# Optimization experiments

Measured on AMD Instinct MI355X. Metric: run time of the kernel, lower is better.

## Reference

```python
import jax, jax.numpy as jnp
import numpy as np

EPS = 1e-5

def layer_norm(x, g, b):
    m = jnp.mean(x, axis=-1, keepdims=True)
    v = jnp.mean((x - m) ** 2, axis=-1, keepdims=True)
    return (x - m) / jnp.sqrt(v + EPS) * g + b

def setup_inputs() -> dict:
    key = jax.random.key(0)
    ks = jax.random.split(key, 12)
    B, S, D, H = 8, 2048, 1024, 2048
    std = 0.02
    inp = {
        "x_embeddings": jax.random.normal(ks[0], (B, S, D), jnp.float32),
        # weights stored [in, out]; torch Linear computes x @ W.T + b
        "wq": jax.random.normal(ks[1], (D, D), jnp.float32) * std,
        "bq": jnp.zeros((D,), jnp.float32),
        "wk": jax.random.normal(ks[2], (D, D), jnp.float32) * std,
        "bk": jnp.zeros((D,), jnp.float32),
        "wv": jax.random.normal(ks[3], (D, D), jnp.float32) * std,
        "bv": jnp.zeros((D,), jnp.float32),
        "w0": jax.random.normal(ks[4], (D, D), jnp.float32) * std,
        "b0": jnp.zeros((D,), jnp.float32),
        "w1": jax.random.normal(ks[5], (D, H), jnp.float32) * std,
        "b1": jnp.zeros((H,), jnp.float32),
        "ln_g": jnp.ones((H,), jnp.float32),
        "ln_b": jnp.zeros((H,), jnp.float32),
        "w2": jax.random.normal(ks[6], (H, D), jnp.float32) * std,
        "b2": jnp.zeros((D,), jnp.float32),
        "n1_g": jnp.ones((D,), jnp.float32),
        "n1_b": jnp.zeros((D,), jnp.float32),
        "n2_g": jnp.ones((D,), jnp.float32),
        "n2_b": jnp.zeros((D,), jnp.float32),
    }
    return inp

def reference(x_embeddings, wq, bq, wk, bk, wv, bv, w0, b0, w1, b1, ln_g, ln_b, w2, b2, n1_g, n1_b, n2_g, n2_b):
    x = x_embeddings
    q = x @ wq + bq  # [B,S,D]
    k = x @ wk + bk
    v = x @ wv + bv
    # NOTE: original has NO 1/sqrt(d) scaling and NO causal mask in forward
    scores = jnp.einsum("bsd,btd->bst", q, k)
    probs = jax.nn.softmax(scores, axis=-1)
    attn = jnp.einsum("bst,btd->bsd", probs, v)
    e = layer_norm(x + attn, n1_g, n1_b) @ w0 + b0
    # MLP: Linear -> LeakyReLU -> LayerNorm(2048) -> Dropout(eval: identity) -> Linear
    h = jax.nn.leaky_relu(e @ w1 + b1, negative_slope=0.01)
    h = layer_norm(h, ln_g, ln_b)
    logits = h @ w2 + b2
    return layer_norm(jax.nn.leaky_relu(logits + e, negative_slope=0.01), n2_g, n2_b)
```

## Files before the change

kernel.cpp:

```cpp
#include <hip/hip_runtime.h>
#include <cstdint>
#include <cmath>

typedef unsigned short u16;
typedef __attribute__((ext_vector_type(4))) float f32x4;
typedef __attribute__((ext_vector_type(8))) _Float16 f16x8;

#define GPTR(p) ((__attribute__((address_space(1))) void*)(uintptr_t)(p))
#define LPTR(p) ((__attribute__((address_space(3))) void*)(uint32_t)(uintptr_t)(p))

__device__ __forceinline__ u16 f2h(float f) {
  const _Float16 h = (_Float16)f;
  return __builtin_bit_cast(u16, h);
}
__device__ __forceinline__ float h2f(u16 v) {
  return (float)__builtin_bit_cast(_Float16, v);
}

__global__ __launch_bounds__(256) void fill_kernel(float* __restrict__ p, float v, long n) {
  const long i = (long)blockIdx.x * 256 + threadIdx.x;
  if (i < n) p[i] = v;
}

__global__ __launch_bounds__(256) void cvt_kernel(const float* __restrict__ src, u16* __restrict__ dst) {
  const long i = ((long)blockIdx.x * 256 + threadIdx.x) * 8;
  const float4 a = *(const float4*)&src[i];
  const float4 b = *(const float4*)&src[i + 4];
  uint4 o;
  o.x = (uint32_t)f2h(a.x) | ((uint32_t)f2h(a.y) << 16);
  o.y = (uint32_t)f2h(a.z) | ((uint32_t)f2h(a.w) << 16);
  o.z = (uint32_t)f2h(b.x) | ((uint32_t)f2h(b.y) << 16);
  o.w = (uint32_t)f2h(b.z) | ((uint32_t)f2h(b.w) << 16);
  *(uint4*)&dst[i] = o;
}

__global__ void transpose_kernel(const float* __restrict__ src, u16* __restrict__ dst, int R, int C) {
  __shared__ float tile[32][33];
  const int bx = blockIdx.x * 32, by = blockIdx.y * 32;
  const int tx = threadIdx.x, ty = threadIdx.y;
#pragma unroll
  for (int i = 0; i < 32; i += 8) tile[ty + i][tx] = src[(long)(by + ty + i) * C + bx + tx];
  __syncthreads();
#pragma unroll
  for (int i = 0; i < 32; i += 8) dst[(long)(bx + ty + i) * R + by + tx] = f2h(tile[tx][ty + i]);
}

__global__ __launch_bounds__(256) void gemm_f16(
    const u16* __restrict__ A, const u16* __restrict__ Bt,
    float* __restrict__ outF, u16* __restrict__ outH, u16* __restrict__ outT,
    const float* __restrict__ bias, const u16* __restrict__ resH,
    int act,
    int K, int lda, int ldb, int ldc, int ldt,
    long strA, long strB, long strC, long strT)
{
  __shared__ alignas(16) u16 sA[128 * 32];
  __shared__ alignas(16) u16 sB[128 * 32];

  const int tid = threadIdx.x;
  const int lane = tid & 63;
  const int wv = tid >> 6;
  const int wr = wv >> 1, wc = wv & 1;
  const int fr = lane & 15, fg = lane >> 4;

  const int z = blockIdx.z;
  const int rowBase = blockIdx.y * 128;
  const int colBase = blockIdx.x * 128;

  const u16* Ab = A + (long)z * strA;
  const u16* Bb = Bt + (long)z * strB;

  const int srow = wv * 32 + (lane >> 2);
  const int scol = (lane & 3) * 8;
  const u16* gA0 = Ab + (long)(rowBase + srow) * lda + scol;
  const u16* gA1 = gA0 + (long)16 * lda;
  const u16* gB0 = Bb + (long)(colBase + srow) * ldb + scol;
  const u16* gB1 = gB0 + (long)16 * ldb;
  u16* lA0 = &sA[wv * 1024];
  u16* lA1 = lA0 + 512;
  u16* lB0 = &sB[wv * 1024];
  u16* lB1 = lB0 + 512;

  f32x4 acc[4][4];
#pragma unroll
  for (int m = 0; m < 4; ++m)
#pragma unroll
    for (int n = 0; n < 4; ++n) acc[m][n] = (f32x4){0.f, 0.f, 0.f, 0.f};

  const int nk = K >> 5;
  __builtin_amdgcn_global_load_lds(GPTR(gA0), LPTR(lA0), 16, 0, 0);
  __builtin_amdgcn_global_load_lds(GPTR(gA1), LPTR(lA1), 16, 0, 0);
  __builtin_amdgcn_global_load_lds(GPTR(gB0), LPTR(lB0), 16, 0, 0);
  __builtin_amdgcn_global_load_lds(GPTR(gB1), LPTR(lB1), 16, 0, 0);

  for (int kt = 0; kt < nk; ++kt) {
    asm volatile("s_waitcnt vmcnt(0)" ::: "memory");
    __syncthreads();

    f16x8 af[4], bfr[4];
#pragma unroll
    for (int m = 0; m < 4; ++m) af[m] = *(const f16x8*)&sA[(wr * 64 + m * 16 + fr) * 32 + fg * 8];
#pragma unroll
    for (int n = 0; n < 4; ++n) bfr[n] = *(const f16x8*)&sB[(wc * 64 + n * 16 + fr) * 32 + fg * 8];
#pragma unroll
    for (int m = 0; m < 4; ++m)
#pragma unroll
      for (int n = 0; n < 4; ++n)
        acc[m][n] = __builtin_amdgcn_mfma_f32_16x16x32_f16(af[m], bfr[n], acc[m][n], 0, 0, 0);

    if (kt + 1 < nk) {
      __syncthreads();
      const long o = (long)(kt + 1) * 32;
      __builtin_amdgcn_global_load_lds(GPTR(gA0 + o), LPTR(lA0), 16, 0, 0);
      __builtin_amdgcn_global_load_lds(GPTR(gA1 + o), LPTR(lA1), 16, 0, 0);
      __builtin_amdgcn_global_load_lds(GPTR(gB0 + o), LPTR(lB0), 16, 0, 0);
      __builtin_amdgcn_global_load_lds(GPTR(gB1 + o), LPTR(lB1), 16, 0, 0);
    }
  }

  float* oF = outF ? outF + (long)z * strC : nullptr;
  u16* oH = outH ? outH + (long)z * strC : nullptr;
  u16* oT = outT ? outT + (long)z * strT : nullptr;
  const u16* rH = resH ? resH + (long)z * strC : nullptr;

#pragma unroll
  for (int n = 0; n < 4; ++n) {
    const int col = colBase + wc * 64 + n * 16 + fr;
    const float bc = bias ? bias[col] : 0.f;
#pragma unroll
    for (int m = 0; m < 4; ++m) {
      const int row0 = rowBase + wr * 64 + m * 16 + fg * 4;
      float y[4];
#pragma unroll
      for (int j = 0; j < 4; ++j) {
        float val = acc[m][n][j] + bc;
        if (rH) val += h2f(rH[(long)(row0 + j) * ldc + col]);
        if (act) val = val > 0.f ? val : 0.01f * val;
        y[j] = val;
        if (oF) oF[(long)(row0 + j) * ldc + col] = val;
        if (oH) oH[(long)(row0 + j) * ldc + col] = f2h(val);
      }
      if (oT) {
        uint2 pk;
        pk.x = (uint32_t)f2h(y[0]) | ((uint32_t)f2h(y[1]) << 16);
        pk.y = (uint32_t)f2h(y[2]) | ((uint32_t)f2h(y[3]) << 16);
        *(uint2*)&oT[(long)col * ldt + row0] = pk;
      }
    }
  }
}

__global__ __launch_bounds__(256) void softmax_kernel(u16* __restrict__ buf) {
  __shared__ float red[16];
  const long base = (long)blockIdx.x * 2048;
  const int t = threadIdx.x, lane = t & 63, wv = t >> 6;
  const uint4 a = *(const uint4*)&buf[base + t * 8];
  float v[8] = {h2f((u16)(a.x & 0xFFFF)), h2f((u16)(a.x >> 16)),
                h2f((u16)(a.y & 0xFFFF)), h2f((u16)(a.y >> 16)),
                h2f((u16)(a.z & 0xFFFF)), h2f((u16)(a.z >> 16)),
                h2f((u16)(a.w & 0xFFFF)), h2f((u16)(a.w >> 16))};
  float mx = v[0];
#pragma unroll
  for (int i = 1; i < 8; ++i) mx = fmaxf(mx, v[i]);
#pragma unroll
  for (int o = 32; o; o >>= 1) mx = fmaxf(mx, __shfl_xor(mx, o));
  if (lane == 0) red[wv] = mx;
  __syncthreads();
  mx = fmaxf(fmaxf(red[0], red[1]), fmaxf(red[2], red[3]));
  float s = 0.f;
#pragma unroll
  for (int i = 0; i < 8; ++i) { v[i] = __expf(v[i] - mx); s += v[i]; }
#pragma unroll
  for (int o = 32; o; o >>= 1) s += __shfl_xor(s, o);
  if (lane == 0) red[8 + wv] = s;
  __syncthreads();
  const float inv = 1.f / (red[8] + red[9] + red[10] + red[11]);
  uint4 o4;
  o4.x = (uint32_t)f2h(v[0] * inv) | ((uint32_t)f2h(v[1] * inv) << 16);
  o4.y = (uint32_t)f2h(v[2] * inv) | ((uint32_t)f2h(v[3] * inv) << 16);
  o4.z = (uint32_t)f2h(v[4] * inv) | ((uint32_t)f2h(v[5] * inv) << 16);
  o4.w = (uint32_t)f2h(v[6] * inv) | ((uint32_t)f2h(v[7] * inv) << 16);
  *(uint4*)&buf[base + t * 8] = o4;
}

template <int W>
__global__ __launch_bounds__(256) void ln_kernel(
    const float* __restrict__ inF, const u16* __restrict__ inH, const float* __restrict__ resF,
    const float* __restrict__ gam, const float* __restrict__ bet,
    float* __restrict__ outF, u16* __restrict__ outH)
{
  constexpr int NV = W / 1024;
  __shared__ float red[16];
  const long base = (long)blockIdx.x * W;
  const int t = threadIdx.x, lane = t & 63, wv = t >> 6;
  float v[NV * 4];
  float s = 0.f, ss = 0.f;
#pragma unroll
  for (int c = 0; c < NV; ++c) {
    const int idx = (t + c * 256) * 4;
    float4 a;
    if (inF) a = *(const float4*)&inF[base + idx];
    else {
      const uint2 r = *(const uint2*)&inH[base + idx];
      a.x = h2f((u16)(r.x & 0xFFFF)); a.y = h2f((u16)(r.x >> 16));
      a.z = h2f((u16)(r.y & 0xFFFF)); a.w = h2f((u16)(r.y >> 16));
    }
    if (resF) {
      const float4 r4 = *(const float4*)&resF[base + idx];
      a.x += r4.x; a.y += r4.y; a.z += r4.z; a.w += r4.w;
    }
    v[c * 4 + 0] = a.x; v[c * 4 + 1] = a.y; v[c * 4 + 2] = a.z; v[c * 4 + 3] = a.w;
    s += a.x + a.y + a.z + a.w;
    ss += a.x * a.x + a.y * a.y + a.z * a.z + a.w * a.w;
  }
#pragma unroll
  for (int o = 32; o; o >>= 1) { s += __shfl_xor(s, o); ss += __shfl_xor(ss, o); }
  if (lane == 0) { red[wv] = s; red[8 + wv] = ss; }
  __syncthreads();
  s = red[0] + red[1] + red[2] + red[3];
  ss = red[8] + red[9] + red[10] + red[11];
  const float mean = s * (1.f / W);
  const float rstd = rsqrtf(ss * (1.f / W) - mean * mean + 1e-5f);
#pragma unroll
  for (int c = 0; c < NV; ++c) {
    const int idx = (t + c * 256) * 4;
    const float4 g4 = *(const float4*)&gam[idx];
    const float4 b4 = *(const float4*)&bet[idx];
    const float y0 = (v[c * 4 + 0] - mean) * rstd * g4.x + b4.x;
    const float y1 = (v[c * 4 + 1] - mean) * rstd * g4.y + b4.y;
    const float y2 = (v[c * 4 + 2] - mean) * rstd * g4.z + b4.z;
    const float y3 = (v[c * 4 + 3] - mean) * rstd * g4.w + b4.w;
    if (outF) { float4 o4 = {y0, y1, y2, y3}; *(float4*)&outF[base + idx] = o4; }
    if (outH) {
      uint2 p;
      p.x = (uint32_t)f2h(y0) | ((uint32_t)f2h(y1) << 16);
      p.y = (uint32_t)f2h(y2) | ((uint32_t)f2h(y3) << 16);
      *(uint2*)&outH[base + idx] = p;
    }
  }
}

extern "C" void kernel_launch(void* const* d_in, const int* in_sizes, int n_in,
                              void* d_out, int out_size, void* d_ws, size_t ws_size,
                              hipStream_t stream) {
  const float* x   = (const float*)d_in[0];
  const float* wq  = (const float*)d_in[1];
  const float* bq  = (const float*)d_in[2];
  const float* wk  = (const float*)d_in[3];
  const float* bk  = (const float*)d_in[4];
  const float* wv  = (const float*)d_in[5];
  const float* bv  = (const float*)d_in[6];
  const float* w0  = (const float*)d_in[7];
  const float* b0  = (const float*)d_in[8];
  const float* w1  = (const float*)d_in[9];
  const float* b1  = (const float*)d_in[10];
  const float* lng = (const float*)d_in[11];
  const float* lnb = (const float*)d_in[12];
  const float* w2  = (const float*)d_in[13];
  const float* b2  = (const float*)d_in[14];
  const float* n1g = (const float*)d_in[15];
  const float* n1b = (const float*)d_in[16];
  const float* n2g = (const float*)d_in[17];
  const float* n2b = (const float*)d_in[18];
  float* out = (float*)d_out;

  const size_t NEED = 251658240u;
  if (ws_size < NEED) {
    int k = (int)(ws_size >> 25); if (k > 60) k = 60;
    const float sentinel = ldexpf(1.0f, k + 4);
    fill_kernel<<<dim3((out_size + 255) / 256), dim3(256), 0, stream>>>(out, sentinel, out_size);
    return;
  }
  char* ws = (char*)d_ws;
  u16* xb    = (u16*)(ws);
  u16* sc    = (u16*)(ws);
  u16* hb    = (u16*)(ws);
  u16* qb    = (u16*)(ws + 67108864);
  u16* attnb = qb;
  u16* kb    = (u16*)(ws + 100663296);
  u16* tb    = kb;
  u16* vT    = (u16*)(ws + 134217728);
  u16* eb    = vT;
  u16* hraw  = (u16*)(ws + 167772160);
  float* uF  = (float*)(ws + 67108864);
  u16* wqT   = (u16*)(ws + 234881024);
  u16* wkT   = (u16*)(ws + 236978176);
  u16* wvT   = (u16*)(ws + 239075328);
  u16* w0T   = (u16*)(ws + 241172480);
  u16* w1T   = (u16*)(ws + 243269632);
  u16* w2T   = (u16*)(ws + 247463936);

  const dim3 b256(256);
  const dim3 tblk(32, 8);

  cvt_kernel<<<dim3(8192), b256, 0, stream>>>(x, xb);
  transpose_kernel<<<dim3(32, 32), tblk, 0, stream>>>(wq, wqT, 1024, 1024);
  transpose_kernel<<<dim3(32, 32), tblk, 0, stream>>>(wk, wkT, 1024, 1024);
  transpose_kernel<<<dim3(32, 32), tblk, 0, stream>>>(wv, wvT, 1024, 1024);
  transpose_kernel<<<dim3(32, 32), tblk, 0, stream>>>(w0, w0T, 1024, 1024);
  transpose_kernel<<<dim3(64, 32), tblk, 0, stream>>>(w1, w1T, 1024, 2048);
  transpose_kernel<<<dim3(32, 64), tblk, 0, stream>>>(w2, w2T, 2048, 1024);

  gemm_f16<<<dim3(8, 128, 1), b256, 0, stream>>>(xb, wqT, nullptr, qb, nullptr, bq, nullptr,
      0, 1024, 1024, 1024, 1024, 0, 0, 0, 0, 0);
  gemm_f16<<<dim3(8, 128, 1), b256, 0, stream>>>(xb, wkT, nullptr, kb, nullptr, bk, nullptr,
      0, 1024, 1024, 1024, 1024, 0, 0, 0, 0, 0);
  gemm_f16<<<dim3(8, 128, 1), b256, 0, stream>>>(xb, wvT, nullptr, nullptr, vT, bv, nullptr,
      0, 1024, 1024, 1024, 1024, 16384, 0, 0, 0, 0);

  gemm_f16<<<dim3(16, 16, 8), b256, 0, stream>>>(qb, kb, nullptr, sc, nullptr, nullptr, nullptr,
      0, 1024, 1024, 1024, 2048, 0, 2097152, 2097152, 4194304, 0);

  softmax_kernel<<<dim3(16384), b256, 0, stream>>>(sc);

  gemm_f16<<<dim3(8, 16, 8), b256, 0, stream>>>(sc, vT, nullptr, attnb, nullptr, nullptr, nullptr,
      0, 2048, 2048, 16384, 1024, 0, 4194304, 2048, 2097152, 0);

  ln_kernel<1024><<<dim3(16384), b256, 0, stream>>>(nullptr, attnb, x, n1g, n1b, nullptr, tb);

  gemm_f16<<<dim3(8, 128, 1), b256, 0, stream>>>(tb, w0T, nullptr, eb, nullptr, b0, nullptr,
      0, 1024, 1024, 1024, 1024, 0, 0, 0, 0, 0);

  gemm_f16<<<dim3(16, 128, 1), b256, 0, stream>>>(eb, w1T, nullptr, hraw, nullptr, b1, nullptr,
      1, 1024, 1024, 1024, 2048, 0, 0, 0, 0, 0);

  ln_kernel<2048><<<dim3(16384), b256, 0, stream>>>(nullptr, hraw, nullptr, lng, lnb, nullptr, hb);

  gemm_f16<<<dim3(8, 128, 1), b256, 0, stream>>>(hb, w2T, uF, nullptr, nullptr, b2, eb,
      1, 2048, 2048, 2048, 1024, 0, 0, 0, 0, 0);

  ln_kernel<1024><<<dim3(16384), b256, 0, stream>>>(uF, nullptr, nullptr, n2g, n2b, out, nullptr);
}
```

Measured before the change: 1.029 ms.

## Rewrite GEMM with 256x128 tiles, K=64 steps, triple-buffered swizzled LDS

Replaces the 128x128, K=32, single-buffered GEMM with a 512-thread kernel that computes 256x128 tiles. It steps K by 64, triple-buffers global-to-LDS loads two stages ahead, and XOR-swizzles the LDS layout to avoid bank conflicts. The goal is to hide global load latency behind MFMA work and reduce LDS bank conflicts and barrier overhead per FLOP, with s_setprio raising the MFMA phase's priority. The costs are about 144KB of LDS per block and more complex waitcnt logic. The epilogue's wr/wc mapping with 8 waves and a 256-row tile must match, but that part is not visible here.

```diff
diff --git a/kernel.cpp b/kernel.cpp
--- a/kernel.cpp
+++ b/kernel.cpp
@@ -45,7 +45,7 @@
   for (int i = 0; i < 32; i += 8) dst[(long)(bx + ty + i) * R + by + tx] = f2h(tile[tx][ty + i]);
 }
 
-__global__ __launch_bounds__(256) void gemm_f16(
+__global__ __launch_bounds__(512, 2) void gemm256(
     const u16* __restrict__ A, const u16* __restrict__ Bt,
     float* __restrict__ outF, u16* __restrict__ outH, u16* __restrict__ outT,
     const float* __restrict__ bias, const u16* __restrict__ resH,
@@ -53,32 +53,28 @@
     int K, int lda, int ldb, int ldc, int ldt,
     long strA, long strB, long strC, long strT)
 {
-  __shared__ alignas(16) u16 sA[128 * 32];
-  __shared__ alignas(16) u16 sB[128 * 32];
+  __shared__ alignas(16) u16 lds[73728];
 
   const int tid = threadIdx.x;
   const int lane = tid & 63;
-  const int wv = tid >> 6;
-  const int wr = wv >> 1, wc = wv & 1;
+  const int wid = tid >> 6;
+  const int wr = wid >> 1, wc = wid & 1;
   const int fr = lane & 15, fg = lane >> 4;
 
   const int z = blockIdx.z;
-  const int rowBase = blockIdx.y * 128;
+  const int rowBase = blockIdx.y * 256;
   const int colBase = blockIdx.x * 128;
 
   const u16* Ab = A + (long)z * strA;
   const u16* Bb = Bt + (long)z * strB;
 
-  const int srow = wv * 32 + (lane >> 2);
-  const int scol = (lane & 3) * 8;
-  const u16* gA0 = Ab + (long)(rowBase + srow) * lda + scol;
-  const u16* gA1 = gA0 + (long)16 * lda;
-  const u16* gB0 = Bb + (long)(colBase + srow) * ldb + scol;
-  const u16* gB1 = gB0 + (long)16 * ldb;
-  u16* lA0 = &sA[wv * 1024];
-  u16* lA1 = lA0 + 512;
-  u16* lB0 = &sB[wv * 1024];
-  u16* lB1 = lB0 + 512;
+  const int sr = tid >> 3;
+  const int jsrc = (tid & 7) ^ (sr & 7);
+  const u16* gA = Ab + (long)(rowBase + sr) * lda + jsrc * 8;
+  const u16* gB = Bb + (long)(colBase + sr) * ldb + jsrc * 8;
+  u16* lA = &lds[tid * 8];
+  u16* lB = &lds[49152 + tid * 8];
+  const int nk = K >> 6;
 
   f32x4 acc[4][4];
 #pragma unroll
@@ -86,36 +82,68 @@
 #pragma unroll
     for (int n = 0; n < 4; ++n) acc[m][n] = (f32x4){0.f, 0.f, 0.f, 0.f};
 
-  const int nk = K >> 5;
-  __builtin_amdgcn_global_load_lds(GPTR(gA0), LPTR(lA0), 16, 0, 0);
-  __builtin_amdgcn_global_load_lds(GPTR(gA1), LPTR(lA1), 16, 0, 0);
-  __builtin_amdgcn_global_load_lds(GPTR(gB0), LPTR(lB0), 16, 0, 0);
-  __builtin_amdgcn_global_load_lds(GPTR(gB1), LPTR(lB1), 16, 0, 0);
-
-  for (int kt = 0; kt < nk; ++kt) {
-    asm volatile("s_waitcnt vmcnt(0)" ::: "memory");
-    __syncthreads();
-
-    f16x8 af[4], bfr[4];
-#pragma unroll
-    for (int m = 0; m < 4; ++m) af[m] = *(const f16x8*)&sA[(wr * 64 + m * 16 + fr) * 32 + fg * 8];
-#pragma unroll
-    for (int n = 0; n < 4; ++n) bfr[n] = *(const f16x8*)&sB[(wc * 64 + n * 16 + fr) * 32 + fg * 8];
+#define STAGE(kt, b)                                                                          \
+  do {                                                                                        \
+    const long ko = (long)(kt) * 64;                                                          \
+    _Pragma("unroll")                                                                         \
+    for (int i = 0; i < 4; ++i)                                                               \
+      __builtin_amdgcn_global_load_lds(GPTR(gA + ko + (long)i * 64 * lda),                    \
+                                       LPTR(lA + (b) * 16384 + i * 4096), 16, 0, 0);          \
+    _Pragma("unroll")                                                                         \
+    for (int i = 0; i < 2; ++i)                                                               \
+      __builtin_amdgcn_global_load_lds(GPTR(gB + ko + (long)i * 64 * ldb),                    \
+                                       LPTR(lB + (b) * 8192 + i * 4096), 16, 0, 0);           \
+  } while (0)
+
+  STAGE(0, 0);
+  STAGE(1, 1);
+
+  int rb = 0;
+  for (int t = 0; t < nk; ++t) {
+    if (t + 1 < nk) asm volatile("s_waitcnt vmcnt(6)" ::: "memory");
+    else            asm volatile("s_waitcnt vmcnt(0)" ::: "memory");
+    __builtin_amdgcn_s_barrier();
+    __builtin_amdgcn_sched_barrier(0);
+
+    const int abase = rb * 16384;
+    const int bbase = 49152 + rb * 8192;
+
+    f16x8 af[4][2], bf[4][2];
 #pragma unroll
     for (int m = 0; m < 4; ++m)
 #pragma unroll
-      for (int n = 0; n < 4; ++n)
-        acc[m][n] = __builtin_amdgcn_mfma_f32_16x16x32_f16(af[m], bfr[n], acc[m][n], 0, 0, 0);
-
-    if (kt + 1 < nk) {
-      __syncthreads();
-      const long o = (long)(kt + 1) * 32;
-      __builtin_amdgcn_global_load_lds(GPTR(gA0 + o), LPTR(lA0), 16, 0, 0);
-      __builtin_amdgcn_global_load_lds(GPTR(gA1 + o), LPTR(lA1), 16, 0, 0);
-      __builtin_amdgcn_global_load_lds(GPTR(gB0 + o), LPTR(lB0), 16, 0, 0);
-      __builtin_amdgcn_global_load_lds(GPTR(gB1 + o), LPTR(lB1), 16, 0, 0);
-    }
-  }
+      for (int kk = 0; kk < 2; ++kk) {
+        const int jp = (kk * 4 + fg) ^ (fr & 7);
+        af[m][kk] = *(const f16x8*)&lds[abase + (wr * 64 + m * 16 + fr) * 64 + jp * 8];
+      }
+#pragma unroll
+    for (int n = 0; n < 4; ++n)
+#pragma unroll
+      for (int kk = 0; kk < 2; ++kk) {
+        const int jp = (kk * 4 + fg) ^ (fr & 7);
+        bf[n][kk] = *(const f16x8*)&lds[bbase + (wc * 64 + n * 16 + fr) * 64 + jp * 8];
+      }
+    asm volatile("s_waitcnt lgkmcnt(0)" ::: "memory");
+    __builtin_amdgcn_s_barrier();
+    __builtin_amdgcn_sched_barrier(0);
+    if (t + 2 < nk) {
+      const int wbuf = rb == 0 ? 2 : rb - 1;
+      STAGE(t + 2, wbuf);
+    }
+
+    __builtin_amdgcn_s_setprio(1);
+#pragma unroll
+    for (int m = 0; m < 4; ++m)
+#pragma unroll
+      for (int n = 0; n < 4; ++n) {
+        acc[m][n] = __builtin_amdgcn_mfma_f32_16x16x32_f16(af[m][0], bf[n][0], acc[m][n], 0, 0, 0);
+        acc[m][n] = __builtin_amdgcn_mfma_f32_16x16x32_f16(af[m][1], bf[n][1], acc[m][n], 0, 0, 0);
+      }
+    __builtin_amdgcn_s_setprio(0);
+
+    rb = rb == 2 ? 0 : rb + 1;
+  }
+#undef STAGE
 
   float* oF = outF ? outF + (long)z * strC : nullptr;
   u16* oH = outH ? outH + (long)z * strC : nullptr;
@@ -290,6 +318,7 @@
   u16* w2T   = (u16*)(ws + 247463936);
 
   const dim3 b256(256);
+  const dim3 b512(512);
   const dim3 tblk(32, 8);
 
   cvt_kernel<<<dim3(8192), b256, 0, stream>>>(x, xb);
@@ -300,32 +329,32 @@
   transpose_kernel<<<dim3(64, 32), tblk, 0, stream>>>(w1, w1T, 1024, 2048);
   transpose_kernel<<<dim3(32, 64), tblk, 0, stream>>>(w2, w2T, 2048, 1024);
 
-  gemm_f16<<<dim3(8, 128, 1), b256, 0, stream>>>(xb, wqT, nullptr, qb, nullptr, bq, nullptr,
+  gemm256<<<dim3(8, 64, 1), b512, 0, stream>>>(xb, wqT, nullptr, qb, nullptr, bq, nullptr,
       0, 1024, 1024, 1024, 1024, 0, 0, 0, 0, 0);
-  gemm_f16<<<dim3(8, 128, 1), b256, 0, stream>>>(xb, wkT, nullptr, kb, nullptr, bk, nullptr,
+  gemm256<<<dim3(8, 64, 1), b512, 0, stream>>>(xb, wkT, nullptr, kb, nullptr, bk, nullptr,
       0, 1024, 1024, 1024, 1024, 0, 0, 0, 0, 0);
-  gemm_f16<<<dim3(8, 128, 1), b256, 0, stream>>>(xb, wvT, nullptr, nullptr, vT, bv, nullptr,
+  gemm256<<<dim3(8, 64, 1), b512, 0, stream>>>(xb, wvT, nullptr, nullptr, vT, bv, nullptr,
       0, 1024, 1024, 1024, 1024, 16384, 0, 0, 0, 0);
 
-  gemm_f16<<<dim3(16, 16, 8), b256, 0, stream>>>(qb, kb, nullptr, sc, nullptr, nullptr, nullptr,
+  gemm256<<<dim3(16, 8, 8), b512, 0, stream>>>(qb, kb, nullptr, sc, nullptr, nullptr, nullptr,
       0, 1024, 1024, 1024, 2048, 0, 2097152, 2097152, 4194304, 0);
 
   softmax_kernel<<<dim3(16384), b256, 0, stream>>>(sc);
 
-  gemm_f16<<<dim3(8, 16, 8), b256, 0, stream>>>(sc, vT, nullptr, attnb, nullptr, nullptr, nullptr,
+  gemm256<<<dim3(8, 8, 8), b512, 0, stream>>>(sc, vT, nullptr, attnb, nullptr, nullptr, nullptr,
       0, 2048, 2048, 16384, 1024, 0, 4194304, 2048, 2097152, 0);
 
   ln_kernel<1024><<<dim3(16384), b256, 0, stream>>>(nullptr, attnb, x, n1g, n1b, nullptr, tb);
 
-  gemm_f16<<<dim3(8, 128, 1), b256, 0, stream>>>(tb, w0T, nullptr, eb, nullptr, b0, nullptr,
+  gemm256<<<dim3(8, 64, 1), b512, 0, stream>>>(tb, w0T, nullptr, eb, nullptr, b0, nullptr,
       0, 1024, 1024, 1024, 1024, 0, 0, 0, 0, 0);
 
-  gemm_f16<<<dim3(16, 128, 1), b256, 0, stream>>>(eb, w1T, nullptr, hraw, nullptr, b1, nullptr,
+  gemm256<<<dim3(16, 64, 1), b512, 0, stream>>>(eb, w1T, nullptr, hraw, nullptr, b1, nullptr,
       1, 1024, 1024, 1024, 2048, 0, 0, 0, 0, 0);
 
   ln_kernel<2048><<<dim3(16384), b256, 0, stream>>>(nullptr, hraw, nullptr, lng, lnb, nullptr, hb);
 
-  gemm_f16<<<dim3(8, 128, 1), b256, 0, stream>>>(hb, w2T, uF, nullptr, nullptr, b2, eb,
+  gemm256<<<dim3(8, 64, 1), b512, 0, stream>>>(hb, w2T, uF, nullptr, nullptr, b2, eb,
       1, 2048, 2048, 2048, 1024, 0, 0, 0, 0, 0);
 
   ln_kernel<1024><<<dim3(16384), b256, 0, stream>>>(uF, nullptr, nullptr, n2g, n2b, out, nullptr);
```

Measured after the change: 904.0 us. 12.1% less time.
